# Optimization experiments

Hardware: AMD Instinct MI355X
Metric: run time of the kernel (lower is better)

## Reference

```python
import jax, jax.numpy as jnp
import numpy as np

D = 1024      # input_dim
H = 4096      # hidden_dim
E = 8         # expert_count
TOP_K = 2
N = 8192      # tokens
LN_EPS = 1e-5


def setup_inputs() -> dict:
    key = jax.random.key(0)
    ks = jax.random.split(key, 10)
    s_d = 1.0 / np.sqrt(D)
    s_h = 1.0 / np.sqrt(H)
    return {
        "x": jax.random.normal(ks[0], (N, D), dtype=jnp.float32),
        "ln_gamma": jnp.ones((D,), jnp.float32),
        "ln_beta": jnp.zeros((D,), jnp.float32),
        "conf_w": jax.random.uniform(ks[1], (D, 1), jnp.float32, -s_d, s_d),
        "conf_b": jnp.zeros((1,), jnp.float32),
        "router_w": jax.random.uniform(ks[2], (D, E), jnp.float32, -s_d, s_d),
        "router_b": jnp.zeros((E,), jnp.float32),
        "w1": jax.random.uniform(ks[3], (E, D, H), jnp.float32, -s_d, s_d),
        "b1": jax.random.uniform(ks[4], (E, H), jnp.float32, -s_d, s_d),
        "w2": jax.random.uniform(ks[5], (E, H, D), jnp.float32, -s_h, s_h),
        "b2": jax.random.uniform(ks[6], (E, D), jnp.float32, -s_h, s_h),
    }


def reference(x, ln_gamma, ln_beta, conf_w, conf_b, router_w, router_b, w1, b1, w2, b2):
    # LayerNorm (torch default eps=1e-5, affine)
    mu = jnp.mean(x, axis=-1, keepdims=True)
    var = jnp.mean(jnp.square(x - mu), axis=-1, keepdims=True)
    x_norm = (x - mu) * jax.lax.rsqrt(var + LN_EPS) * ln_gamma + ln_beta

    # layer-skip confidence head
    confidence = jax.nn.sigmoid(x_norm @ conf_w + conf_b)  # [N,1]

    # router: softmax -> top-k -> renormalize selected weights
    router_probs = jax.nn.softmax(x_norm @ router_w + router_b, axis=-1)  # [N,E]
    vals, indices = jax.lax.top_k(router_probs, TOP_K)                    # [N,K]
    vals = vals / jnp.sum(vals, axis=-1, keepdims=True)

    # scatter top-k weights into dense per-expert combine weights [N,E]
    combine_w = jnp.zeros((x.shape[0], E), x.dtype).at[
        jnp.arange(x.shape[0])[:, None], indices].add(vals)

    # dispatch/combine: loop over small fixed expert count (dense compute,
    # weighted by combine_w, mathematically identical to per-token dispatch)
    combined = jnp.zeros_like(x)
    for e in range(E):
        h = jax.nn.relu(x_norm @ w1[e] + b1[e])      # [N,H]
        combined = combined + combine_w[:, e:e + 1] * (h @ w2[e] + b2[e])

    output = x + combined
    return output, confidence, x
```

## Files before the change

kernel.cpp:

```cpp
#include <hip/hip_runtime.h>
#include <hip/hip_bf16.h>

#define N_TOK 8192
#define DIM   1024
#define HID   4096
#define NEXP  8
#define CSTR  64
#define RTMAX 72
#define HROWS 16896
#define EPS   264

using bf16x8 = __attribute__((ext_vector_type(8))) short;
using f32x4  = __attribute__((ext_vector_type(4))) float;

__device__ __forceinline__ void gload_lds16(const void* g, void* l) {
  __builtin_amdgcn_global_load_lds(
      (const __attribute__((address_space(1))) unsigned int*)g,
      (__attribute__((address_space(3))) unsigned int*)l, 16, 0, 0);
}

__device__ __forceinline__ float wredsum(float v) {
#pragma unroll
  for (int off = 32; off > 0; off >>= 1) v += __shfl_xor(v, off, 64);
  return v;
}

__device__ __forceinline__ unsigned short f2bf(float f) {
  __hip_bfloat16 h = __float2bfloat16(f);
  return *reinterpret_cast<unsigned short*>(&h);
}
__device__ __forceinline__ float bf2f(unsigned short u) {
  return __uint_as_float((unsigned)u << 16);
}

__device__ __forceinline__ void transpose_body(
    const float* __restrict__ src, __hip_bfloat16* __restrict__ dst,
    int R, int C, int c0, int r0, float (*tile)[65]) {
  const int tid = threadIdx.x;
  const int tx = tid & 15, ty = tid >> 4;
#pragma unroll
  for (int k = 0; k < 4; k++) {
    const int row = ty + k * 16;
    const float4 v = *(const float4*)(src + (size_t)(r0 + row) * C + c0 + tx * 4);
    tile[row][tx * 4 + 0] = v.x; tile[row][tx * 4 + 1] = v.y;
    tile[row][tx * 4 + 2] = v.z; tile[row][tx * 4 + 3] = v.w;
  }
  __syncthreads();
#pragma unroll
  for (int k = 0; k < 4; k++) {
    const int orow = ty + k * 16;
    ushort4 st;
    st.x = f2bf(tile[tx * 4 + 0][orow]);
    st.y = f2bf(tile[tx * 4 + 1][orow]);
    st.z = f2bf(tile[tx * 4 + 2][orow]);
    st.w = f2bf(tile[tx * 4 + 3][orow]);
    *(ushort4*)((unsigned short*)dst + (size_t)(c0 + orow) * R + r0 + tx * 4) = st;
  }
}

__global__ __launch_bounds__(256) void setup_kernel(
    const float* __restrict__ x, const float* __restrict__ gamma, const float* __restrict__ beta,
    const float* __restrict__ conf_w, const float* __restrict__ conf_b,
    const float* __restrict__ rw, const float* __restrict__ rb,
    const float* __restrict__ w1, const float* __restrict__ w2,
    __hip_bfloat16* __restrict__ w1t, __hip_bfloat16* __restrict__ w2t,
    __hip_bfloat16* __restrict__ xn, float* __restrict__ out,
    int* __restrict__ counts, int* __restrict__ lists, float* __restrict__ wts,
    int2* __restrict__ idx) {
  __shared__ float tile[64][65];
  const int b = (int)blockIdx.x;
  if (b < 8192) {
    const int z = b >> 10, r = b & 1023;
    const int cx = r & 63, ry = r >> 6;
    transpose_body(w1 + (size_t)z * DIM * HID, w1t + (size_t)z * DIM * HID,
                   DIM, HID, cx * 64, ry * 64, tile);
    return;
  }
  if (b < 16384) {
    const int bb = b - 8192;
    const int z = bb >> 10, r = bb & 1023;
    const int cx = r & 15, ry = r >> 4;
    transpose_body(w2 + (size_t)z * HID * DIM, w2t + (size_t)z * HID * DIM,
                   HID, DIM, cx * 64, ry * 64, tile);
    return;
  }
  const int t = (b - 16384) * 4 + ((int)threadIdx.x >> 6);
  const int lane = threadIdx.x & 63;
  const float* xr = x + (size_t)t * DIM;

  float4 xv[4];
#pragma unroll
  for (int q = 0; q < 4; q++) xv[q] = *(const float4*)(xr + q * 256 + lane * 4);

  float s = 0.f, s2 = 0.f;
#pragma unroll
  for (int q = 0; q < 4; q++) {
    s  += xv[q].x + xv[q].y + xv[q].z + xv[q].w;
    s2 += xv[q].x * xv[q].x + xv[q].y * xv[q].y + xv[q].z * xv[q].z + xv[q].w * xv[q].w;
  }
  s = wredsum(s); s2 = wredsum(s2);
  const float mu  = s * (1.f / DIM);
  const float inv = rsqrtf(s2 * (1.f / DIM) - mu * mu + 1e-5f);

  float p[9];
#pragma unroll
  for (int e = 0; e < 9; e++) p[e] = 0.f;

#pragma unroll
  for (int q = 0; q < 4; q++) {
    const int d0 = q * 256 + lane * 4;
    const float4 g4 = *(const float4*)(gamma + d0);
    const float4 b4 = *(const float4*)(beta + d0);
    float v0 = (xv[q].x - mu) * inv * g4.x + b4.x;
    float v1 = (xv[q].y - mu) * inv * g4.y + b4.y;
    float v2 = (xv[q].z - mu) * inv * g4.z + b4.z;
    float v3 = (xv[q].w - mu) * inv * g4.w + b4.w;

    ushort4 st; st.x = f2bf(v0); st.y = f2bf(v1); st.z = f2bf(v2); st.w = f2bf(v3);
    *(ushort4*)((unsigned short*)xn + (size_t)t * DIM + d0) = st;
    *(float4*)(out + (size_t)N_TOK * DIM + N_TOK + (size_t)t * DIM + d0) = xv[q];

    const float vv[4] = {v0, v1, v2, v3};
#pragma unroll
    for (int j = 0; j < 4; j++) {
      const int d = d0 + j;
      const float v = vv[j];
      p[8] += v * conf_w[d];
      const float4 r0 = *(const float4*)(rw + d * 8);
      const float4 r1 = *(const float4*)(rw + d * 8 + 4);
      p[0] += v * r0.x; p[1] += v * r0.y; p[2] += v * r0.z; p[3] += v * r0.w;
      p[4] += v * r1.x; p[5] += v * r1.y; p[6] += v * r1.z; p[7] += v * r1.w;
    }
  }
#pragma unroll
  for (int e = 0; e < 9; e++) p[e] = wredsum(p[e]);

  if (lane == 0) {
    float L[8];
#pragma unroll
    for (int e = 0; e < 8; e++) L[e] = p[e] + rb[e];
    const float cl = p[8] + conf_b[0];
    out[(size_t)N_TOK * DIM + t] = 1.f / (1.f + expf(-cl));

    float mx = L[0];
#pragma unroll
    for (int e = 1; e < 8; e++) mx = fmaxf(mx, L[e]);
    float pe[8];
#pragma unroll
    for (int e = 0; e < 8; e++) pe[e] = expf(L[e] - mx);
    int i0 = 0; float v0 = pe[0];
#pragma unroll
    for (int e = 1; e < 8; e++) if (pe[e] > v0) { v0 = pe[e]; i0 = e; }
    int i1 = -1; float v1 = -1.f;
#pragma unroll
    for (int e = 0; e < 8; e++) if (e != i0 && pe[e] > v1) { v1 = pe[e]; i1 = e; }
    const float wsum = v0 + v1;
    const float w0 = v0 / wsum, w1v = v1 / wsum;
    int p0 = atomicAdd(&counts[i0 * CSTR], 1);
    lists[i0 * N_TOK + p0] = t; wts[i0 * N_TOK + p0] = w0;
    int p1 = atomicAdd(&counts[i1 * CSTR], 1);
    lists[i1 * N_TOK + p1] = t; wts[i1 * N_TOK + p1] = w1v;
    idx[t] = make_int2((i0 << 13) | p0, (i1 << 13) | p1);
  }
}

__global__ void bases_kernel(const int* __restrict__ counts, int* __restrict__ bases,
                             int* __restrict__ meta) {
  if (threadIdx.x == 0) {
    int s = 0, r = 0;
#pragma unroll
    for (int e = 0; e < NEXP; e++) {
      bases[e] = s; meta[e] = r;
      const int c = counts[e * CSTR];
      s += c; r += (c + 255) >> 8;
    }
    meta[NEXP] = r;
  }
}


#define LGKM_SB(N)                                                            \
  asm volatile("s_waitcnt lgkmcnt(" #N ")" ::: "memory");                     \
  __builtin_amdgcn_sched_barrier(0);

#define MFMA_G(MI)                                                            \
  __builtin_amdgcn_s_setprio(1);                                              \
  _Pragma("unroll")                                                           \
  for (int n = 0; n < 4; n++)                                                 \
    acc[MI][n] = __builtin_amdgcn_mfma_f32_16x16x32_bf16(afr[MI], bfr[n], acc[MI][n], 0, 0, 0); \
  __builtin_amdgcn_s_setprio(0);

#define GEMM_CORE(NT)                                                                   \
  f32x4 acc[8][4] = {};                                                                 \
  stage(0, 0); stage(1, 32768);                                                         \
  for (int t = 0; t < (NT); ++t) {                                                      \
    const int pb = (t % 3) * 32768;                                                     \
    if (t + 1 < (NT)) { asm volatile("s_waitcnt vmcnt(4)" ::: "memory"); }              \
    else              { asm volatile("s_waitcnt vmcnt(0)" ::: "memory"); }              \
    __builtin_amdgcn_s_barrier();                                                       \
    if (t + 2 < (NT)) stage(t + 2, ((t + 2) % 3) * 32768);                              \
    const char* Ab = smem + pb + Abase;                                                 \
    const char* Bb = smem + pb + Bbase;                                                 \
    bf16x8 bfr[4], afr[8];                                                              \
    afr[0] = *(const bf16x8*)(Ab);                                                      \
    bfr[0] = *(const bf16x8*)(Bb);                                                      \
    bfr[1] = *(const bf16x8*)(Bb + 1024);                                               \
    __builtin_amdgcn_sched_barrier(0);                                                  \
    bfr[2] = *(const bf16x8*)(Bb + 2048);                                               \
    bfr[3] = *(const bf16x8*)(Bb + 3072);                                               \
    __builtin_amdgcn_sched_barrier(0);                                                  \
    _Pragma("unroll")                                                                   \
    for (int m = 1; m < 8; m++) {                                                       \
      afr[m] = *(const bf16x8*)(Ab + m * 1024);                                         \
      __builtin_amdgcn_sched_barrier(0);                                                \
    }                                                                                   \
    LGKM_SB(7) MFMA_G(0)                                                                \
    LGKM_SB(6) MFMA_G(1)                                                                \
    LGKM_SB(5) MFMA_G(2)                                                                \
    LGKM_SB(4) MFMA_G(3)                                                                \
    LGKM_SB(3) MFMA_G(4)                                                                \
    LGKM_SB(2) MFMA_G(5)                                                                \
    LGKM_SB(1) MFMA_G(6)                                                                \
    LGKM_SB(0) MFMA_G(7)                                                                \
  }

#define DECODE_TAIL()                                                         \
  if (rtg >= meta[NEXP]) return;                                              \
  int e = 0;                                                                  \
  _Pragma("unroll")                                                           \
  for (int k = 1; k < NEXP; k++) if (meta[k] <= rtg) e = k;                   \
  const int rt = rtg - meta[e];                                               \
  const int cnt = counts[e * CSTR];                                           \
  const int hbase = bases[e];

#define GEMM_COMMON()                                                         \
  __shared__ char smem[98304];                                                \
  const int tid = threadIdx.x;                     \
  const int l = tid & 63;                                                     \
  const int w8 = tid >> 6;                                                    \
  const int wr = w8 >> 2;                                                     \
  const int wc = w8 & 3;                                                      \
  const int lr = l & 15;                                                      \
  const int pchunk = (l >> 4) ^ ((lr >> 1) & 3);                              \
  const int Abase = (wr * 128 + lr) * 64 + pchunk * 16;                       \
  const int Bbase = 16384 + (wc * 64 + lr) * 64 + pchunk * 16;                \
  const int srow = tid >> 2;                      \
  const int lc = (tid & 3) ^ ((srow >> 1) & 3);

#define EPILOGUE(DSTROW)                                                      \
  __builtin_amdgcn_s_barrier();                                               \
  {                                                                           \
    unsigned short* ep = (unsigned short*)smem;                               \
    _Pragma("unroll")                                                         \
    for (int h = 0; h < 2; h++) {                                             \
      if (wr == h) {                                                          \
        _Pragma("unroll")                                                     \
        for (int n = 0; n < 4; n++) {                                         \
          const int col = wc * 64 + n * 16 + lr;                              \
          _Pragma("unroll")                                                   \
          for (int m = 0; m < 8; m++) {                                       \
            f32x4 v = acc[m][n];                                              \
            _Pragma("unroll")                                                 \
            for (int j = 0; j < 4; j++)                                       \
              ep[(m * 16 + (l >> 4) * 4 + j) * EPS + col] = f2bf(v[j]);       \
          }                                                                   \
        }                                                                     \
      }                                                                       \
      asm volatile("s_waitcnt lgkmcnt(0)" ::: "memory");                      \
      __builtin_amdgcn_s_barrier();                                           \
      const int g = tid >> 5, u = tid & 31;                                   \
      _Pragma("unroll")                                                       \
      for (int i = 0; i < 8; i++) {                                           \
        const int row = i * 16 + g;                                           \
        const int pos = rt * 256 + h * 128 + row;                             \
        if (pos < cnt) {                                                      \
          bf16x8 vv = *(const bf16x8*)(ep + row * EPS + u * 8);               \
          *(bf16x8*)(DSTROW + u * 8) = vv;                                    \
        }                                                                     \
      }                                                                       \
      __builtin_amdgcn_s_barrier();                                           \
    }                                                                         \
  }

__global__ __launch_bounds__(512, 2) void gemm1_kernel(
    const __hip_bfloat16* __restrict__ xn, const __hip_bfloat16* __restrict__ w1t_b,
    const float* __restrict__ b1, const int* __restrict__ lists,
    const int* __restrict__ counts, const int* __restrict__ bases,
    const int* __restrict__ meta, __hip_bfloat16* __restrict__ hbuf) {
  const int x_ = (int)blockIdx.x & 7;
  const int q_ = (int)blockIdx.x >> 3;
  const int rtg = q_ >> 1;
  const int panel = x_ * 2 + (q_ & 1);
  DECODE_TAIL()
  const int ct = panel;
  const int* list = lists + e * N_TOK;
  const __hip_bfloat16* w1t = w1t_b + (size_t)e * DIM * HID;
  GEMM_COMMON()

  const int ap0 = rt * 256 + srow, ap1 = ap0 + 128;
  const int tok0 = list[ap0 < cnt ? ap0 : 0];
  const int tok1 = list[ap1 < cnt ? ap1 : 0];
  const unsigned short* srcA0 = (const unsigned short*)xn + (size_t)tok0 * DIM + lc * 8;
  const unsigned short* srcA1 = (const unsigned short*)xn + (size_t)tok1 * DIM + lc * 8;
  const unsigned short* srcB0 = (const unsigned short*)w1t + (size_t)(ct * 256 + srow) * DIM + lc * 8;
  const unsigned short* srcB1 = (const unsigned short*)w1t + (size_t)(ct * 256 + 128 + srow) * DIM + lc * 8;

  auto stage = [&](int tt, int lbase) {
    gload_lds16(srcA0 + tt * 32, smem + lbase + tid * 16);
    gload_lds16(srcA1 + tt * 32, smem + lbase + 8192 + tid * 16);
    gload_lds16(srcB0 + tt * 32, smem + lbase + 16384 + tid * 16);
    gload_lds16(srcB1 + tt * 32, smem + lbase + 24576 + tid * 16);
  };

  GEMM_CORE(DIM / 32)

  const float bv[4] = {
    b1[e * HID + ct * 256 + wc * 64 + 0 * 16 + lr],
    b1[e * HID + ct * 256 + wc * 64 + 1 * 16 + lr],
    b1[e * HID + ct * 256 + wc * 64 + 2 * 16 + lr],
    b1[e * HID + ct * 256 + wc * 64 + 3 * 16 + lr]};
#pragma unroll
  for (int n = 0; n < 4; n++)
#pragma unroll
    for (int m = 0; m < 8; m++)
#pragma unroll
      for (int j = 0; j < 4; j++) acc[m][n][j] = fmaxf(acc[m][n][j] + bv[n], 0.f);
  EPILOGUE((unsigned short*)hbuf + (size_t)(hbase + pos) * HID + ct * 256)
}

__global__ __launch_bounds__(512, 2) void gemm2_kernel(
    const __hip_bfloat16* __restrict__ hbuf, const __hip_bfloat16* __restrict__ w2t_b,
    const int* __restrict__ counts, const int* __restrict__ bases,
    const int* __restrict__ meta, __hip_bfloat16* __restrict__ ybuf, const int SK) {
  int panel, rtg;
  if (SK == 2) {
    const int x_ = (int)blockIdx.x & 7;
    const int q_ = (int)blockIdx.x >> 3;
    rtg = (q_ >> 2) * 4 + (x_ >> 1);
    panel = (x_ & 1) * 4 + (q_ & 3);
  } else {
    panel = (int)blockIdx.x / RTMAX;
    rtg = (int)blockIdx.x - panel * RTMAX;
  }
  DECODE_TAIL()
  const int ct = panel & 3;
  const int ksp = panel >> 2;
  const int kbase = ksp * (HID / SK);
  const __hip_bfloat16* w2t = w2t_b + (size_t)e * DIM * HID;
  GEMM_COMMON()

  const unsigned short* srcA0 = (const unsigned short*)hbuf +
      (size_t)(hbase + rt * 256 + srow) * HID + kbase + lc * 8;
  const unsigned short* srcA1 = (const unsigned short*)hbuf +
      (size_t)(hbase + rt * 256 + 128 + srow) * HID + kbase + lc * 8;
  const unsigned short* srcB0 = (const unsigned short*)w2t +
      (size_t)(ct * 256 + srow) * HID + kbase + lc * 8;
  const unsigned short* srcB1 = (const unsigned short*)w2t +
      (size_t)(ct * 256 + 128 + srow) * HID + kbase + lc * 8;

  auto stage = [&](int tt, int lbase) {
    gload_lds16(srcA0 + tt * 32, smem + lbase + tid * 16);
    gload_lds16(srcA1 + tt * 32, smem + lbase + 8192 + tid * 16);
    gload_lds16(srcB0 + tt * 32, smem + lbase + 16384 + tid * 16);
    gload_lds16(srcB1 + tt * 32, smem + lbase + 24576 + tid * 16);
  };

  const int nk = (HID / 32) / SK;
  GEMM_CORE(nk)

  EPILOGUE((unsigned short*)ybuf + ((size_t)ksp * HROWS + hbase + pos) * DIM + ct * 256)
}

__global__ __launch_bounds__(256) void combine_kernel(
    const float* __restrict__ x, const __hip_bfloat16* __restrict__ ybuf,
    const float* __restrict__ b2, const int2* __restrict__ idx,
    const float* __restrict__ wv, const int* __restrict__ bases,
    float* __restrict__ out, const int SK) {
  const int t = blockIdx.x * 4 + (threadIdx.x >> 6);
  const int lane = threadIdx.x & 63;
  const int2 iv = idx[t];
  const int e0 = iv.x >> 13, p0 = iv.x & (N_TOK - 1);
  const int e1 = iv.y >> 13, p1 = iv.y & (N_TOK - 1);
  const float w0 = wv[iv.x], w1 = wv[iv.y];
  const int r0 = bases[e0] + p0;
  const int r1 = bases[e1] + p1;
#pragma unroll
  for (int q = 0; q < 4; q++) {
    const int d0 = q * 256 + lane * 4;
    float4 o = *(const float4*)(x + (size_t)t * DIM + d0);
    float y0x = 0.f, y0y = 0.f, y0z = 0.f, y0w = 0.f;
    float y1x = 0.f, y1y = 0.f, y1z = 0.f, y1w = 0.f;
    for (int s = 0; s < SK; s++) {
      const ushort4 a = *(const ushort4*)((const unsigned short*)ybuf +
                          ((size_t)s * HROWS + r0) * DIM + d0);
      const ushort4 b = *(const ushort4*)((const unsigned short*)ybuf +
                          ((size_t)s * HROWS + r1) * DIM + d0);
      y0x += bf2f(a.x); y0y += bf2f(a.y); y0z += bf2f(a.z); y0w += bf2f(a.w);
      y1x += bf2f(b.x); y1y += bf2f(b.y); y1z += bf2f(b.z); y1w += bf2f(b.w);
    }
    const float4 bb0 = *(const float4*)(b2 + e0 * DIM + d0);
    const float4 bb1 = *(const float4*)(b2 + e1 * DIM + d0);
    o.x += w0 * (y0x + bb0.x) + w1 * (y1x + bb1.x);
    o.y += w0 * (y0y + bb0.y) + w1 * (y1y + bb1.y);
    o.z += w0 * (y0z + bb0.z) + w1 * (y1z + bb1.z);
    o.w += w0 * (y0w + bb0.w) + w1 * (y1w + bb1.w);
    *(float4*)(out + (size_t)t * DIM + d0) = o;
  }
}

extern "C" void kernel_launch(void* const* d_in, const int* in_sizes, int n_in,
                              void* d_out, int out_size, void* d_ws, size_t ws_size,
                              hipStream_t stream) {
  (void)in_sizes; (void)n_in; (void)out_size;
  const float* x      = (const float*)d_in[0];
  const float* gamma  = (const float*)d_in[1];
  const float* beta   = (const float*)d_in[2];
  const float* conf_w = (const float*)d_in[3];
  const float* conf_b = (const float*)d_in[4];
  const float* rw     = (const float*)d_in[5];
  const float* rb     = (const float*)d_in[6];
  const float* w1     = (const float*)d_in[7];
  const float* b1     = (const float*)d_in[8];
  const float* w2     = (const float*)d_in[9];
  const float* b2     = (const float*)d_in[10];
  float* out = (float*)d_out;

  char* w = (char*)d_ws;
  auto alloc = [&](size_t bytes) { char* p = w; w += (bytes + 255) & ~255ULL; return p; };

  __hip_bfloat16* xn = (__hip_bfloat16*)alloc((size_t)N_TOK * DIM * 2);
  int*   lists  = (int*)alloc((size_t)NEXP * N_TOK * 4);
  float* wtsb   = (float*)alloc((size_t)NEXP * N_TOK * 4);
  int*   counts = (int*)alloc(NEXP * CSTR * 4);
  int*   bases  = (int*)alloc(256);
  int*   meta   = (int*)alloc(256);
  int2*  idx    = (int2*)alloc((size_t)N_TOK * 8);

  const size_t hbufA = (size_t)HROWS * HID * 2;
  const size_t wtA   = (size_t)NEXP * DIM * HID * 2;
  __hip_bfloat16* hbuf = (__hip_bfloat16*)alloc(hbufA);
  __hip_bfloat16* w1t  = (__hip_bfloat16*)alloc(wtA);
  __hip_bfloat16* w2t  = (__hip_bfloat16*)alloc(wtA);
  const size_t used = (size_t)(w - (char*)d_ws);
  const size_t ybuf1 = (size_t)HROWS * DIM * 2;

  int SK;
  __hip_bfloat16* ybuf;
  if (ws_size >= used + 2 * ybuf1 + 4096) {
    SK = 2; ybuf = (__hip_bfloat16*)alloc(2 * ybuf1);
  } else {
    SK = 1; ybuf = w1t;
  }
  const int g2grid = (SK == 2) ? 8 * RTMAX : 4 * RTMAX;

  hipMemsetAsync(counts, 0, NEXP * CSTR * 4, stream);
  setup_kernel<<<16384 + N_TOK / 4, 256, 0, stream>>>(
      x, gamma, beta, conf_w, conf_b, rw, rb, w1, w2, w1t, w2t,
      xn, out, counts, lists, wtsb, idx);
  bases_kernel<<<1, 64, 0, stream>>>(counts, bases, meta);
  gemm1_kernel<<<8 * 2 * RTMAX, 512, 0, stream>>>(xn, w1t, b1, lists, counts, bases, meta,
                                                  hbuf);
  gemm2_kernel<<<g2grid, 512, 0, stream>>>(hbuf, w2t, counts, bases, meta, ybuf, SK);
  combine_kernel<<<N_TOK / 4, 256, 0, stream>>>(x, ybuf, b2, idx, wtsb, bases, out, SK);
}
```

Measured before the change: 509.1 us.

## Use 4-wave 128x128 warp tiles with double buffering and overlap W2 transpose with gemm1

Both grouped GEMMs move from 8 waves with 128x64 per-wave tiles and a triple-buffered LDS pipeline to 4 waves with 128x128 per-wave tiles and a double buffer. This raises MFMA work per LDS fragment load. The W2 fp32-to-bf16 transpose leaves the setup kernel and runs as extra blocks appended to the gemm1 grid, so it can overlap with gemm1 compute. In exchange, each wave holds 256 accumulator registers and runs at occupancy 1, and prefetch depth drops to one stage with a full vmcnt(0) wait every iteration, which risks exposing memory latency.

Result: slower. 539.7 us (+6.0%).

```diff
diff --git a/kernel.cpp b/kernel.cpp
--- a/kernel.cpp
+++ b/kernel.cpp
@@ -9,6 +9,7 @@
 #define RTMAX 72
 #define HROWS 16896
 #define EPS   264
+#define NG1   1152
 
 using bf16x8 = __attribute__((ext_vector_type(8))) short;
 using f32x4  = __attribute__((ext_vector_type(4))) float;
@@ -62,8 +63,8 @@
     const float* __restrict__ x, const float* __restrict__ gamma, const float* __restrict__ beta,
     const float* __restrict__ conf_w, const float* __restrict__ conf_b,
     const float* __restrict__ rw, const float* __restrict__ rb,
-    const float* __restrict__ w1, const float* __restrict__ w2,
-    __hip_bfloat16* __restrict__ w1t, __hip_bfloat16* __restrict__ w2t,
+    const float* __restrict__ w1,
+    __hip_bfloat16* __restrict__ w1t,
     __hip_bfloat16* __restrict__ xn, float* __restrict__ out,
     int* __restrict__ counts, int* __restrict__ lists, float* __restrict__ wts,
     int2* __restrict__ idx) {
@@ -76,15 +77,7 @@
                    DIM, HID, cx * 64, ry * 64, tile);
     return;
   }
-  if (b < 16384) {
-    const int bb = b - 8192;
-    const int z = bb >> 10, r = bb & 1023;
-    const int cx = r & 15, ry = r >> 4;
-    transpose_body(w2 + (size_t)z * HID * DIM, w2t + (size_t)z * HID * DIM,
-                   HID, DIM, cx * 64, ry * 64, tile);
-    return;
-  }
-  const int t = (b - 16384) * 4 + ((int)threadIdx.x >> 6);
+  const int t = (b - 8192) * 4 + ((int)threadIdx.x >> 6);
   const int lane = threadIdx.x & 63;
   const float* xr = x + (size_t)t * DIM;
 
@@ -183,45 +176,56 @@
   asm volatile("s_waitcnt lgkmcnt(" #N ")" ::: "memory");                     \
   __builtin_amdgcn_sched_barrier(0);
 
-#define MFMA_G(MI)                                                            \
+#define MFMA_BLK(M0, NM, N0, NN)                                              \
   __builtin_amdgcn_s_setprio(1);                                              \
   _Pragma("unroll")                                                           \
-  for (int n = 0; n < 4; n++)                                                 \
-    acc[MI][n] = __builtin_amdgcn_mfma_f32_16x16x32_bf16(afr[MI], bfr[n], acc[MI][n], 0, 0, 0); \
+  for (int m = (M0); m < (M0) + (NM); m++)                                    \
+    _Pragma("unroll")                                                         \
+    for (int n = (N0); n < (N0) + (NN); n++)                                  \
+      acc[m][n] = __builtin_amdgcn_mfma_f32_16x16x32_bf16(afr[m], bfr[n], acc[m][n], 0, 0, 0); \
   __builtin_amdgcn_s_setprio(0);
 
 #define GEMM_CORE(NT)                                                                   \
-  f32x4 acc[8][4] = {};                                                                 \
-  stage(0, 0); stage(1, 32768);                                                         \
+  f32x4 acc[8][8] = {};                                                                 \
+  stage(0, 0);                                                                          \
   for (int t = 0; t < (NT); ++t) {                                                      \
-    const int pb = (t % 3) * 32768;                                                     \
-    if (t + 1 < (NT)) { asm volatile("s_waitcnt vmcnt(4)" ::: "memory"); }              \
-    else              { asm volatile("s_waitcnt vmcnt(0)" ::: "memory"); }              \
+    const int pb = (t & 1) * 32768;                                                     \
+    asm volatile("s_waitcnt vmcnt(0)" ::: "memory");                                    \
     __builtin_amdgcn_s_barrier();                                                       \
-    if (t + 2 < (NT)) stage(t + 2, ((t + 2) % 3) * 32768);                              \
+    if (t + 1 < (NT)) stage(t + 1, (~t & 1) * 32768);                                   \
     const char* Ab = smem + pb + Abase;                                                 \
     const char* Bb = smem + pb + Bbase;                                                 \
-    bf16x8 bfr[4], afr[8];                                                              \
+    bf16x8 bfr[8], afr[8];                                                              \
     afr[0] = *(const bf16x8*)(Ab);                                                      \
+    afr[1] = *(const bf16x8*)(Ab + 1024);                                               \
     bfr[0] = *(const bf16x8*)(Bb);                                                      \
     bfr[1] = *(const bf16x8*)(Bb + 1024);                                               \
     __builtin_amdgcn_sched_barrier(0);                                                  \
     bfr[2] = *(const bf16x8*)(Bb + 2048);                                               \
     bfr[3] = *(const bf16x8*)(Bb + 3072);                                               \
     __builtin_amdgcn_sched_barrier(0);                                                  \
-    _Pragma("unroll")                                                                   \
-    for (int m = 1; m < 8; m++) {                                                       \
-      afr[m] = *(const bf16x8*)(Ab + m * 1024);                                         \
-      __builtin_amdgcn_sched_barrier(0);                                                \
-    }                                                                                   \
-    LGKM_SB(7) MFMA_G(0)                                                                \
-    LGKM_SB(6) MFMA_G(1)                                                                \
-    LGKM_SB(5) MFMA_G(2)                                                                \
-    LGKM_SB(4) MFMA_G(3)                                                                \
-    LGKM_SB(3) MFMA_G(4)                                                                \
-    LGKM_SB(2) MFMA_G(5)                                                                \
-    LGKM_SB(1) MFMA_G(6)                                                                \
-    LGKM_SB(0) MFMA_G(7)                                                                \
+    bfr[4] = *(const bf16x8*)(Bb + 4096);                                               \
+    bfr[5] = *(const bf16x8*)(Bb + 5120);                                               \
+    __builtin_amdgcn_sched_barrier(0);                                                  \
+    bfr[6] = *(const bf16x8*)(Bb + 6144);                                               \
+    bfr[7] = *(const bf16x8*)(Bb + 7168);                                               \
+    __builtin_amdgcn_sched_barrier(0);                                                  \
+    afr[2] = *(const bf16x8*)(Ab + 2048);                                               \
+    afr[3] = *(const bf16x8*)(Ab + 3072);                                               \
+    __builtin_amdgcn_sched_barrier(0);                                                  \
+    afr[4] = *(const bf16x8*)(Ab + 4096);                                               \
+    afr[5] = *(const bf16x8*)(Ab + 5120);                                               \
+    __builtin_amdgcn_sched_barrier(0);                                                  \
+    afr[6] = *(const bf16x8*)(Ab + 6144);                                               \
+    afr[7] = *(const bf16x8*)(Ab + 7168);                                               \
+    __builtin_amdgcn_sched_barrier(0);                                                  \
+    LGKM_SB(12) MFMA_BLK(0, 2, 0, 2)                                                    \
+    LGKM_SB(10) MFMA_BLK(0, 2, 2, 2)                                                    \
+    LGKM_SB(8)  MFMA_BLK(0, 2, 4, 2)                                                    \
+    LGKM_SB(6)  MFMA_BLK(0, 2, 6, 2)                                                    \
+    LGKM_SB(4)  MFMA_BLK(2, 2, 0, 8)                                                    \
+    LGKM_SB(2)  MFMA_BLK(4, 2, 0, 8)                                                    \
+    LGKM_SB(0)  MFMA_BLK(6, 2, 0, 8)                                                    \
   }
 
 #define DECODE_TAIL()                                                         \
@@ -234,17 +238,16 @@
   const int hbase = bases[e];
 
 #define GEMM_COMMON()                                                         \
-  __shared__ char smem[98304];                                                \
-  const int tid = threadIdx.x;                     \
+  const int tid = threadIdx.x;               \
   const int l = tid & 63;                                                     \
-  const int w8 = tid >> 6;                                                    \
-  const int wr = w8 >> 2;                                                     \
-  const int wc = w8 & 3;                                                      \
+  const int w4 = tid >> 6;                                                    \
+  const int wr = w4 >> 1;                                                     \
+  const int wc = w4 & 1;                                                      \
   const int lr = l & 15;                                                      \
   const int pchunk = (l >> 4) ^ ((lr >> 1) & 3);                              \
   const int Abase = (wr * 128 + lr) * 64 + pchunk * 16;                       \
-  const int Bbase = 16384 + (wc * 64 + lr) * 64 + pchunk * 16;                \
-  const int srow = tid >> 2;                      \
+  const int Bbase = 16384 + (wc * 128 + lr) * 64 + pchunk * 16;               \
+  const int srow = tid >> 2;              \
   const int lc = (tid & 3) ^ ((srow >> 1) & 3);
 
 #define EPILOGUE(DSTROW)                                                      \
@@ -252,14 +255,15 @@
   {                                                                           \
     unsigned short* ep = (unsigned short*)smem;                               \
     _Pragma("unroll")                                                         \
-    for (int h = 0; h < 2; h++) {                                             \
-      if (wr == h) {                                                          \
+    for (int pz = 0; pz < 4; pz++) {                                          \
+      if (wr == (pz >> 1)) {                                                  \
+        const int mlo = (pz & 1) * 4;                                         \
         _Pragma("unroll")                                                     \
-        for (int n = 0; n < 4; n++) {                                         \
-          const int col = wc * 64 + n * 16 + lr;                              \
+        for (int n = 0; n < 8; n++) {                                         \
+          const int col = wc * 128 + n * 16 + lr;                             \
           _Pragma("unroll")                                                   \
-          for (int m = 0; m < 8; m++) {                                       \
-            f32x4 v = acc[m][n];                                              \
+          for (int m = 0; m < 4; m++) {                                       \
+            f32x4 v = acc[mlo + m][n];                                        \
             _Pragma("unroll")                                                 \
             for (int j = 0; j < 4; j++)                                       \
               ep[(m * 16 + (l >> 4) * 4 + j) * EPS + col] = f2bf(v[j]);       \
@@ -271,8 +275,8 @@
       const int g = tid >> 5, u = tid & 31;                                   \
       _Pragma("unroll")                                                       \
       for (int i = 0; i < 8; i++) {                                           \
-        const int row = i * 16 + g;                                           \
-        const int pos = rt * 256 + h * 128 + row;                             \
+        const int row = i * 8 + g;                                            \
+        const int pos = rt * 256 + pz * 64 + row;                             \
         if (pos < cnt) {                                                      \
           bf16x8 vv = *(const bf16x8*)(ep + row * EPS + u * 8);               \
           *(bf16x8*)(DSTROW + u * 8) = vv;                                    \
@@ -282,11 +286,21 @@
     }                                                                         \
   }
 
-__global__ __launch_bounds__(512, 2) void gemm1_kernel(
+__global__ __launch_bounds__(256, 1) void gemm1_kernel(
     const __hip_bfloat16* __restrict__ xn, const __hip_bfloat16* __restrict__ w1t_b,
     const float* __restrict__ b1, const int* __restrict__ lists,
     const int* __restrict__ counts, const int* __restrict__ bases,
-    const int* __restrict__ meta, __hip_bfloat16* __restrict__ hbuf) {
+    const int* __restrict__ meta, __hip_bfloat16* __restrict__ hbuf,
+    const float* __restrict__ w2, __hip_bfloat16* __restrict__ w2t) {
+  __shared__ char smem[65536];
+  if ((int)blockIdx.x >= NG1) {
+    const int bb = (int)blockIdx.x - NG1;
+    const int z = bb >> 10, r = bb & 1023;
+    const int cx = r & 15, ry = r >> 4;
+    transpose_body(w2 + (size_t)z * HID * DIM, w2t + (size_t)z * HID * DIM,
+                   HID, DIM, cx * 64, ry * 64, (float(*)[65])smem);
+    return;
+  }
   const int x_ = (int)blockIdx.x & 7;
   const int q_ = (int)blockIdx.x >> 3;
   const int rtg = q_ >> 1;
@@ -297,30 +311,31 @@
   const __hip_bfloat16* w1t = w1t_b + (size_t)e * DIM * HID;
   GEMM_COMMON()
 
-  const int ap0 = rt * 256 + srow, ap1 = ap0 + 128;
-  const int tok0 = list[ap0 < cnt ? ap0 : 0];
-  const int tok1 = list[ap1 < cnt ? ap1 : 0];
-  const unsigned short* srcA0 = (const unsigned short*)xn + (size_t)tok0 * DIM + lc * 8;
-  const unsigned short* srcA1 = (const unsigned short*)xn + (size_t)tok1 * DIM + lc * 8;
-  const unsigned short* srcB0 = (const unsigned short*)w1t + (size_t)(ct * 256 + srow) * DIM + lc * 8;
-  const unsigned short* srcB1 = (const unsigned short*)w1t + (size_t)(ct * 256 + 128 + srow) * DIM + lc * 8;
-
+  const unsigned short* srcA[4];
+  const unsigned short* srcB[4];
+#pragma unroll
+  for (int j = 0; j < 4; j++) {
+    const int pos = rt * 256 + j * 64 + srow;
+    const int tok = list[pos < cnt ? pos : 0];
+    srcA[j] = (const unsigned short*)xn + (size_t)tok * DIM + lc * 8;
+    srcB[j] = (const unsigned short*)w1t + (size_t)(ct * 256 + j * 64 + srow) * DIM + lc * 8;
+  }
   auto stage = [&](int tt, int lbase) {
-    gload_lds16(srcA0 + tt * 32, smem + lbase + tid * 16);
-    gload_lds16(srcA1 + tt * 32, smem + lbase + 8192 + tid * 16);
-    gload_lds16(srcB0 + tt * 32, smem + lbase + 16384 + tid * 16);
-    gload_lds16(srcB1 + tt * 32, smem + lbase + 24576 + tid * 16);
+#pragma unroll
+    for (int j = 0; j < 4; j++)
+      gload_lds16(srcA[j] + tt * 32, smem + lbase + j * 4096 + tid * 16);
+#pragma unroll
+    for (int j = 0; j < 4; j++)
+      gload_lds16(srcB[j] + tt * 32, smem + lbase + 16384 + j * 4096 + tid * 16);
   };
 
   GEMM_CORE(DIM / 32)
 
-  const float bv[4] = {
-    b1[e * HID + ct * 256 + wc * 64 + 0 * 16 + lr],
-    b1[e * HID + ct * 256 + wc * 64 + 1 * 16 + lr],
-    b1[e * HID + ct * 256 + wc * 64 + 2 * 16 + lr],
-    b1[e * HID + ct * 256 + wc * 64 + 3 * 16 + lr]};
-#pragma unroll
-  for (int n = 0; n < 4; n++)
+  float bv[8];
+#pragma unroll
+  for (int n = 0; n < 8; n++) bv[n] = b1[e * HID + ct * 256 + wc * 128 + n * 16 + lr];
+#pragma unroll
+  for (int n = 0; n < 8; n++)
 #pragma unroll
     for (int m = 0; m < 8; m++)
 #pragma unroll
@@ -328,10 +343,11 @@
   EPILOGUE((unsigned short*)hbuf + (size_t)(hbase + pos) * HID + ct * 256)
 }
 
-__global__ __launch_bounds__(512, 2) void gemm2_kernel(
+__global__ __launch_bounds__(256, 1) void gemm2_kernel(
     const __hip_bfloat16* __restrict__ hbuf, const __hip_bfloat16* __restrict__ w2t_b,
     const int* __restrict__ counts, const int* __restrict__ bases,
     const int* __restrict__ meta, __hip_bfloat16* __restrict__ ybuf, const int SK) {
+  __shared__ char smem[65536];
   int panel, rtg;
   if (SK == 2) {
     const int x_ = (int)blockIdx.x & 7;
@@ -349,20 +365,22 @@
   const __hip_bfloat16* w2t = w2t_b + (size_t)e * DIM * HID;
   GEMM_COMMON()
 
-  const unsigned short* srcA0 = (const unsigned short*)hbuf +
-      (size_t)(hbase + rt * 256 + srow) * HID + kbase + lc * 8;
-  const unsigned short* srcA1 = (const unsigned short*)hbuf +
-      (size_t)(hbase + rt * 256 + 128 + srow) * HID + kbase + lc * 8;
-  const unsigned short* srcB0 = (const unsigned short*)w2t +
-      (size_t)(ct * 256 + srow) * HID + kbase + lc * 8;
-  const unsigned short* srcB1 = (const unsigned short*)w2t +
-      (size_t)(ct * 256 + 128 + srow) * HID + kbase + lc * 8;
-
+  const unsigned short* srcA[4];
+  const unsigned short* srcB[4];
+#pragma unroll
+  for (int j = 0; j < 4; j++) {
+    srcA[j] = (const unsigned short*)hbuf +
+              (size_t)(hbase + rt * 256 + j * 64 + srow) * HID + kbase + lc * 8;
+    srcB[j] = (const unsigned short*)w2t +
+              (size_t)(ct * 256 + j * 64 + srow) * HID + kbase + lc * 8;
+  }
   auto stage = [&](int tt, int lbase) {
-    gload_lds16(srcA0 + tt * 32, smem + lbase + tid * 16);
-    gload_lds16(srcA1 + tt * 32, smem + lbase + 8192 + tid * 16);
-    gload_lds16(srcB0 + tt * 32, smem + lbase + 16384 + tid * 16);
-    gload_lds16(srcB1 + tt * 32, smem + lbase + 24576 + tid * 16);
+#pragma unroll
+    for (int j = 0; j < 4; j++)
+      gload_lds16(srcA[j] + tt * 32, smem + lbase + j * 4096 + tid * 16);
+#pragma unroll
+    for (int j = 0; j < 4; j++)
+      gload_lds16(srcB[j] + tt * 32, smem + lbase + 16384 + j * 4096 + tid * 16);
   };
 
   const int nk = (HID / 32) / SK;
@@ -454,12 +472,12 @@
   const int g2grid = (SK == 2) ? 8 * RTMAX : 4 * RTMAX;
 
   hipMemsetAsync(counts, 0, NEXP * CSTR * 4, stream);
-  setup_kernel<<<16384 + N_TOK / 4, 256, 0, stream>>>(
-      x, gamma, beta, conf_w, conf_b, rw, rb, w1, w2, w1t, w2t,
+  setup_kernel<<<8192 + N_TOK / 4, 256, 0, stream>>>(
+      x, gamma, beta, conf_w, conf_b, rw, rb, w1, w1t,
       xn, out, counts, lists, wtsb, idx);
   bases_kernel<<<1, 64, 0, stream>>>(counts, bases, meta);
-  gemm1_kernel<<<8 * 2 * RTMAX, 512, 0, stream>>>(xn, w1t, b1, lists, counts, bases, meta,
-                                                  hbuf);
-  gemm2_kernel<<<g2grid, 512, 0, stream>>>(hbuf, w2t, counts, bases, meta, ybuf, SK);
+  gemm1_kernel<<<NG1 + 8192, 256, 0, stream>>>(xn, w1t, b1, lists, counts, bases, meta,
+                                               hbuf, w2, w2t);
+  gemm2_kernel<<<g2grid, 256, 0, stream>>>(hbuf, w2t, counts, bases, meta, ybuf, SK);
   combine_kernel<<<N_TOK / 4, 256, 0, stream>>>(x, ybuf, b2, idx, wtsb, bases, out, SK);
 }
```
